# Performance work log

Measured on AMD Instinct MI355X. Metric: run time of the kernel, lower is better.

## Reference

```python
import jax, jax.numpy as jnp
import numpy as np
import math

NUM_HEADS = 16
SEGMENT_SIZE = 256
DILATION_RATE = 2


def _hilbert_curve(n):
    if n == 1:
        return [(0, 0)]
    m = n // 2
    sub = _hilbert_curve(m)
    pts = [(y, x) for (x, y) in sub]
    pts += [(x, y + m) for (x, y) in sub]
    pts += [(x + m, y + m) for (x, y) in sub]
    pts += [(m - 1 - y + m, m - 1 - x) for (x, y) in sub]
    return pts


def generate_hilbert_curve_mapping(seq_len):
    grid = 2 ** int(math.ceil(math.log2(math.sqrt(seq_len))))
    pts = _hilbert_curve(grid)
    lin2hil = np.zeros(seq_len, dtype=np.int32)
    for h_idx, (x, y) in enumerate(pts[:seq_len]):
        lin = y * grid + x
        if lin < seq_len:
            lin2hil[lin] = h_idx
    return lin2hil


def setup_inputs() -> dict:
    key = jax.random.key(0)
    k1, k2, k3 = jax.random.split(key, 3)
    B, S, H = 1, 4096, 2048
    scale = H ** -0.5
    x = jax.random.normal(k1, (B, S, H), dtype=jnp.float32)
    w_qkv = jax.random.normal(k2, (3 * H, H), dtype=jnp.float32) * scale
    w_out = jax.random.normal(k3, (H, H), dtype=jnp.float32) * scale
    hilbert_map = jnp.asarray(generate_hilbert_curve_mapping(S))
    return {"x": x, "w_qkv": w_qkv, "w_out": w_out, "hilbert_map": hilbert_map}


def _kv_positions(S, seg, dil):
    # Union of per-segment dilated positions: seg_start + j*dil (< segment end).
    seg_starts = np.arange(0, S, seg)
    within = np.arange(0, seg, dil)
    return jnp.asarray((seg_starts[:, None] + within[None, :]).reshape(-1))


def reference(x, w_qkv, w_out, hilbert_map):
    B, S, H = x.shape
    nh = NUM_HEADS
    hd = H // nh
    qkv = x @ w_qkv.T                              # [B,S,3H]
    qkv = qkv.reshape(B, S, 3, nh, hd).transpose(2, 0, 3, 1, 4)  # [3,B,nh,S,hd]
    q, k, v = qkv[0], qkv[1], qkv[2]

    kv_pos = _kv_positions(S, SEGMENT_SIZE, DILATION_RATE)  # [Nk]
    gathered = hilbert_map[kv_pos]                 # Hilbert-mapped KV indices
    kg = k[:, :, gathered, :]                      # [B,nh,Nk,hd]
    vg = v[:, :, gathered, :]

    scale = 1.0 / jnp.sqrt(jnp.float32(hd))
    scores = jnp.einsum("bhmd,bhnd->bhmn", q, kg) * scale
    p = jax.nn.softmax(scores, axis=-1)
    acc = jnp.einsum("bhmn,bhnd->bhmd", p, vg)     # [B,nh,S,hd]

    # Scatter: out[:, :, hilbert_map[m], :] = acc[:, :, m, :]
    out = jnp.zeros_like(acc).at[:, :, hilbert_map, :].set(acc)
    out = out.transpose(0, 2, 1, 3).reshape(B, S, H)
    return out @ w_out.T
```

## Files before the change

kernel.cpp:

```cpp
#include <hip/hip_runtime.h>
#include <math.h>

#define S_LEN 4096
#define HID   2048
#define NH    16
#define HD    128
#define NKV   2048
#define KT    64
#define QBLK  256
#define NT    (NKV / KT)
#define QSCALE 0.12754103668587426f

typedef __attribute__((ext_vector_type(8))) _Float16 half8;
typedef __attribute__((ext_vector_type(4))) _Float16 half4;
typedef __attribute__((ext_vector_type(2))) __fp16 fp16x2;
typedef __attribute__((ext_vector_type(4))) float f32x4;
typedef __attribute__((ext_vector_type(16))) float f32x16;

#define GLB_AS __attribute__((address_space(1)))
#define LDS_AS __attribute__((address_space(3)))

__device__ __forceinline__ void gload16(const void* g, void* l) {
  __builtin_amdgcn_global_load_lds((GLB_AS const void*)g, (LDS_AS void*)l, 16, 0, 0);
}

__device__ __forceinline__ unsigned pkrtz(float a, float b) {
  union { fp16x2 h; unsigned u; } cv;
  cv.h = __builtin_amdgcn_cvt_pkrtz(a, b);
  return cv.u;
}

__global__ void k_build_idx(const int* __restrict__ hmap, int* __restrict__ gidx) {
  int i = blockIdx.x * 256 + threadIdx.x;
  if (i < NKV) gidx[i] = hmap[2 * i];
}

__global__ void k_cvt_f16(const float* __restrict__ src, _Float16* __restrict__ dst, int n8) {
  int i = blockIdx.x * 256 + threadIdx.x;
  if (i < n8) {
    float4 a = ((const float4*)src)[2 * i];
    float4 b = ((const float4*)src)[2 * i + 1];
    half8 h;
    h[0] = (_Float16)a.x; h[1] = (_Float16)a.y; h[2] = (_Float16)a.z; h[3] = (_Float16)a.w;
    h[4] = (_Float16)b.x; h[5] = (_Float16)b.y; h[6] = (_Float16)b.z; h[7] = (_Float16)b.w;
    ((half8*)dst)[i] = h;
  }
}

template<bool OUT_F32>
__global__ __launch_bounds__(256)
void k_gemm2(const _Float16* __restrict__ A, const _Float16* __restrict__ B,
             void* __restrict__ Cv, int M, int N, int K,
             const int* __restrict__ arow)
{
  __shared__ __align__(16) char Asl[16384];
  __shared__ __align__(16) char Bsl[16384];
  const int tid = threadIdx.x;
  const int w = tid >> 6, lane = tid & 63;
  const int l15 = lane & 15, l4 = lane >> 4;
  const int m0 = blockIdx.y * 128, n0 = blockIdx.x * 128;
  const int wr = w >> 1, wc = w & 1;

  const int srow  = lane >> 3;
  const int kso   = ((lane & 7) ^ srow) * 8;
  const _Float16* Ap[4];
  const _Float16* Bp[4];
#pragma unroll
  for (int q = 0; q < 4; ++q) {
    int arel = m0 + 32 * w + 8 * q + srow;
    int ra = arow ? arow[arel] : arel;
    Ap[q] = A + (size_t)ra * K + kso;
    Bp[q] = B + (size_t)(n0 + 32 * w + 8 * q + srow) * K + kso;
  }

  f32x4 acc[4][4];
#pragma unroll
  for (int i = 0; i < 4; ++i)
#pragma unroll
    for (int j = 0; j < 4; ++j) acc[i][j] = (f32x4){0.f, 0.f, 0.f, 0.f};

#define STAGE_T(k0)                                                  \
  do {                                                               \
    _Pragma("unroll")                                                \
    for (int q = 0; q < 4; ++q) {                                    \
      gload16(Ap[q] + (k0), Asl + (4 * w + q) * 1024 + lane * 16);   \
      gload16(Bp[q] + (k0), Bsl + (4 * w + q) * 1024 + lane * 16);   \
    }                                                                \
  } while (0)

  STAGE_T(0);
  __syncthreads();

  const int nt = K >> 6;
  for (int t = 0; t < nt; ++t) {
    half8 af[4][2], bf[4][2];
#pragma unroll
    for (int mi = 0; mi < 4; ++mi) {
      int row = wr * 64 + mi * 16 + l15;
#pragma unroll
      for (int ks = 0; ks < 2; ++ks)
        af[mi][ks] = *(const half8*)(Asl + row * 128 + (((ks * 4 + l4) ^ (row & 7)) * 16));
    }
#pragma unroll
    for (int ni = 0; ni < 4; ++ni) {
      int row = wc * 64 + ni * 16 + l15;
#pragma unroll
      for (int ks = 0; ks < 2; ++ks)
        bf[ni][ks] = *(const half8*)(Bsl + row * 128 + (((ks * 4 + l4) ^ (row & 7)) * 16));
    }
    __syncthreads();
    if (t + 1 < nt) STAGE_T((t + 1) * 64);
    __builtin_amdgcn_s_setprio(1);
#pragma unroll
    for (int mi = 0; mi < 4; ++mi)
#pragma unroll
      for (int ni = 0; ni < 4; ++ni)
#pragma unroll
        for (int ks = 0; ks < 2; ++ks)
          acc[mi][ni] = __builtin_amdgcn_mfma_f32_16x16x32_f16(af[mi][ks], bf[ni][ks], acc[mi][ni], 0, 0, 0);
    __builtin_amdgcn_s_setprio(0);
    __syncthreads();
  }
#undef STAGE_T

  const int rbase = m0 + wr * 64 + l4 * 4;
  const int cbase = n0 + wc * 64 + l15;
#pragma unroll
  for (int mi = 0; mi < 4; ++mi)
#pragma unroll
    for (int ni = 0; ni < 4; ++ni)
#pragma unroll
      for (int e = 0; e < 4; ++e) {
        size_t idx = (size_t)(rbase + mi * 16 + e) * N + cbase + ni * 16;
        if (OUT_F32) ((float*)Cv)[idx] = acc[mi][ni][e];
        else ((_Float16*)Cv)[idx] = (_Float16)acc[mi][ni][e];
      }
}

__global__ __launch_bounds__(256)
void k_prep(const _Float16* __restrict__ kv, char* __restrict__ kimg,
            char* __restrict__ vtimg)
{
  __shared__ _Float16 Vs[64 * 136];
  const int tid = threadIdx.x;
  const int h = blockIdx.x >> 5;
  const int t = blockIdx.x & 31;
  const size_t ibase = (size_t)blockIdx.x * 16384;

#pragma unroll
  for (int it = 0; it < 4; ++it) {
    int idx = tid + 256 * it;
    int j = idx >> 4, dblk = idx & 15;
    const _Float16* rb = kv + (size_t)(t * KT + j) * (2 * HID) + h * HD + dblk * 8;
    half8 kvv = *(const half8*)rb;
    *(half8*)(kimg + ibase + ((j * 256 + 16 * dblk) ^ ((j & 7) << 4))) = kvv;
    half8 vv = *(const half8*)(rb + HID);
    *(half8*)(&Vs[j * 136 + dblk * 8]) = vv;
  }
  __syncthreads();
#pragma unroll
  for (int it = 0; it < 4; ++it) {
    int idx = tid + 256 * it;
    int jblk = idx >> 7, d = idx & 127;
    half8 o;
#pragma unroll
    for (int q = 0; q < 8; ++q) o[q] = Vs[(jblk * 8 + q) * 136 + d];
    *(half8*)(vtimg + ibase + ((d * 128 + 16 * jblk) ^ ((d & 7) << 4))) = o;
  }
}

__global__ __launch_bounds__(512, 2)
void k_attn4(const _Float16* __restrict__ qmat, const char* __restrict__ kimg,
             const char* __restrict__ vtimg, const int* __restrict__ hmap,
             _Float16* __restrict__ att)
{
  extern __shared__ __align__(16) char lds[];
  const int tid = threadIdx.x;
  const int w = tid >> 6, lane = tid & 63;
  const int l31 = lane & 31;
  const bool hi = (lane >> 5) != 0;
  const int hib = hi ? 1 : 0;
  const int work = (blockIdx.x & 7) * 32 + (blockIdx.x >> 3);
  const int h  = work >> 4;
  const int q0 = (work & 15) * QBLK;

  half8 qf[8];
  {
    const int qrow = q0 + w * 32 + l31;
    const _Float16* qb = qmat + (size_t)qrow * HID + h * HD + hib * 8;
    const _Float16 qs = (_Float16)QSCALE;
#pragma unroll
    for (int dk = 0; dk < 8; ++dk) {
      half8 v = *(const half8*)(qb + 16 * dk);
#pragma unroll
      for (int q = 0; q < 8; ++q) v[q] *= qs;
      qf[dk] = v;
    }
  }

  half8 ones;
#pragma unroll
  for (int q = 0; q < 8; ++q) ones[q] = (_Float16)1.0f;

  const char* kbase = kimg  + (size_t)h * NT * 16384;
  const char* vbase = vtimg + (size_t)h * NT * 16384;

  f32x16 acc[4];
  f32x16 accl;
#pragma unroll
  for (int dt = 0; dt < 4; ++dt)
#pragma unroll
    for (int r = 0; r < 16; ++r) acc[dt][r] = 0.f;
#pragma unroll
  for (int r = 0; r < 16; ++r) accl[r] = 0.f;
  float m = -1e30f;

#define STAGE(buf, t)                                                          \
  do {                                                                         \
    const char* ks_ = kbase + (size_t)(t) * 16384;                             \
    const char* vs_ = vbase + (size_t)(t) * 16384;                             \
    char* d_ = lds + (buf) * 32768;                                            \
    gload16(ks_ + w * 1024 + lane * 16,          d_ + w * 1024);               \
    gload16(ks_ + (8 + w) * 1024 + lane * 16,    d_ + (8 + w) * 1024);         \
    gload16(vs_ + w * 1024 + lane * 16,          d_ + 16384 + w * 1024);       \
    gload16(vs_ + (8 + w) * 1024 + lane * 16,    d_ + 16384 + (8 + w) * 1024); \
  } while (0)

  STAGE(0, 0);
  asm volatile("s_waitcnt vmcnt(0)");
  __syncthreads();

  int cur = 0;
  for (int t = 0; t < NT; ++t) {
    if (t + 1 < NT) STAGE(cur ^ 1, t + 1);
    const char* kl = lds + cur * 32768;
    const char* vl = kl + 16384;

    f32x16 s[2];
    __builtin_amdgcn_s_setprio(1);
#pragma unroll
    for (int jt = 0; jt < 2; ++jt) {
      f32x16 ss;
#pragma unroll
      for (int r = 0; r < 16; ++r) ss[r] = 0.f;
      const int j = jt * 32 + l31;
#pragma unroll
      for (int dk = 0; dk < 8; ++dk) {
        half8 kf = *(const half8*)(kl + j * 256 + ((dk * 32 + hib * 16) ^ ((l31 & 7) << 4)));
        ss = __builtin_amdgcn_mfma_f32_32x32x16_f16(kf, qf[dk], ss, 0, 0, 0);
      }
      s[jt] = ss;
    }
    __builtin_amdgcn_s_setprio(0);

    float vmax = -1e30f;
#pragma unroll
    for (int jt = 0; jt < 2; ++jt)
#pragma unroll
      for (int r = 0; r < 16; ++r) vmax = fmaxf(vmax, s[jt][r]);
    vmax = fmaxf(vmax, __shfl_xor(vmax, 32));

    if (__any(vmax > m + 8.f)) {
      float mn = fmaxf(m, vmax);
      float corr = exp2f(m - mn);
      m = mn;
#pragma unroll
      for (int dt = 0; dt < 4; ++dt)
#pragma unroll
        for (int r = 0; r < 16; ++r) acc[dt][r] *= corr;
#pragma unroll
      for (int r = 0; r < 16; ++r) accl[r] *= corr;
    }

    unsigned P_pk[2][4][2];
#pragma unroll
    for (int jt = 0; jt < 2; ++jt)
#pragma unroll
      for (int rq = 0; rq < 4; ++rq)
#pragma unroll
        for (int h2 = 0; h2 < 2; ++h2) {
          float p0 = exp2f(s[jt][4 * rq + 2 * h2]     - m);
          float p1 = exp2f(s[jt][4 * rq + 2 * h2 + 1] - m);
          P_pk[jt][rq][h2] = pkrtz(p0, p1);
        }

#pragma unroll
    for (int ks = 0; ks < 4; ++ks) {
      const int jt = ks >> 1, k1 = ks & 1;
      unsigned send0 = hi ? P_pk[jt][2 * k1][0]     : P_pk[jt][2 * k1 + 1][0];
      unsigned send1 = hi ? P_pk[jt][2 * k1][1]     : P_pk[jt][2 * k1 + 1][1];
      unsigned recv0 = (unsigned)__shfl_xor((int)send0, 32);
      unsigned recv1 = (unsigned)__shfl_xor((int)send1, 32);
      unsigned self0 = hi ? P_pk[jt][2 * k1 + 1][0] : P_pk[jt][2 * k1][0];
      unsigned self1 = hi ? P_pk[jt][2 * k1 + 1][1] : P_pk[jt][2 * k1][1];
      union { unsigned u[4]; half8 hv; } pf;
      pf.u[0] = hi ? recv0 : self0;
      pf.u[1] = hi ? recv1 : self1;
      pf.u[2] = hi ? self0 : recv0;
      pf.u[3] = hi ? self1 : recv1;
      __builtin_amdgcn_s_setprio(1);
#pragma unroll
      for (int dt = 0; dt < 4; ++dt) {
        const int d = dt * 32 + l31;
        half8 vf = *(const half8*)(vl + d * 128 + ((ks * 32 + hib * 16) ^ ((l31 & 7) << 4)));
        acc[dt] = __builtin_amdgcn_mfma_f32_32x32x16_f16(vf, pf.hv, acc[dt], 0, 0, 0);
      }
      accl = __builtin_amdgcn_mfma_f32_32x32x16_f16(ones, pf.hv, accl, 0, 0, 0);
      __builtin_amdgcn_s_setprio(0);
    }

    asm volatile("s_waitcnt vmcnt(0)");
    __syncthreads();
    cur ^= 1;
  }
#undef STAGE

  const float rl = 1.0f / accl[0];
  const int qrow = q0 + w * 32 + l31;
  const int srow = hmap[qrow];
  _Float16* ob = att + (size_t)srow * HID + h * HD;
#pragma unroll
  for (int dt = 0; dt < 4; ++dt)
#pragma unroll
    for (int rq = 0; rq < 4; ++rq) {
      const int d0 = dt * 32 + 8 * rq + 4 * hib;
      half4 o;
      o[0] = (_Float16)(acc[dt][4 * rq + 0] * rl);
      o[1] = (_Float16)(acc[dt][4 * rq + 1] * rl);
      o[2] = (_Float16)(acc[dt][4 * rq + 2] * rl);
      o[3] = (_Float16)(acc[dt][4 * rq + 3] * rl);
      *(half4*)(ob + d0) = o;
    }
}

extern "C" void kernel_launch(void* const* d_in, const int* in_sizes, int n_in,
                              void* d_out, int out_size, void* d_ws, size_t ws_size,
                              hipStream_t stream)
{
  const float* x     = (const float*)d_in[0];
  const float* w_qkv = (const float*)d_in[1];
  const float* w_out = (const float*)d_in[2];
  const int*   hmap  = (const int*)d_in[3];
  float* out = (float*)d_out;

  char* ws = (char*)d_ws;
  int* gidx = (int*)ws;                                          ws += 8192;
  _Float16* x16    = (_Float16*)ws;
  _Float16* att16  = (_Float16*)ws;                              ws += (size_t)S_LEN * HID * 2;
  _Float16* wqkv16 = (_Float16*)ws;                              ws += (size_t)3 * HID * HID * 2;
  _Float16* wout16 = (_Float16*)ws;                              ws += (size_t)HID * HID * 2;
  _Float16* q16    = (_Float16*)ws;                              ws += (size_t)S_LEN * HID * 2;
  _Float16* kv16   = (_Float16*)ws;                              ws += (size_t)NKV * 2 * HID * 2;
  char* kimg  = ws;                                              ws += (size_t)NH * NT * 16384;
  char* vtimg = ws;

  k_build_idx<<<8, 256, 0, stream>>>(hmap, gidx);

  k_cvt_f16<<<(S_LEN * HID / 8 + 255) / 256, 256, 0, stream>>>(x, x16, S_LEN * HID / 8);
  k_cvt_f16<<<(3 * HID * HID / 8 + 255) / 256, 256, 0, stream>>>(w_qkv, wqkv16, 3 * HID * HID / 8);
  k_cvt_f16<<<(HID * HID / 8 + 255) / 256, 256, 0, stream>>>(w_out, wout16, HID * HID / 8);

  dim3 gq(HID / 128, S_LEN / 128);
  k_gemm2<false><<<gq, 256, 0, stream>>>(x16, wqkv16, q16, S_LEN, HID, HID, nullptr);
  dim3 gkv(2 * HID / 128, NKV / 128);
  k_gemm2<false><<<gkv, 256, 0, stream>>>(x16, wqkv16 + (size_t)HID * HID, kv16,
                                          NKV, 2 * HID, HID, gidx);

  k_prep<<<NH * NT, 256, 0, stream>>>(kv16, kimg, vtimg);

  k_attn4<<<NH * (S_LEN / QBLK), 512, 65536, stream>>>(q16, kimg, vtimg, hmap, att16);

  dim3 go(HID / 128, S_LEN / 128);
  k_gemm2<true><<<go, 256, 0, stream>>>(att16, wout16, out, S_LEN, HID, HID, nullptr);
}
```

Before: 244.3 us.

## Fuse K/V image layout into KV GEMM epilogue and shrink attention blocks

The KV projection GEMM now writes its output straight into the swizzled K image and transposed V image, so the separate k_prep kernel and the kv16 intermediate buffer are gone. The attention kernel is re-tiled to 128 query rows per block with 256 threads, which doubles the grid and changes the LDS staging loop. The row-max reduction is also rewritten as a tree. The risk is that the scattered 2-byte stores in the GEMM epilogue are poorly coalesced, and the smaller attention blocks reuse each K/V tile less.

```diff
diff --git a/kernel.cpp b/kernel.cpp
--- a/kernel.cpp
+++ b/kernel.cpp
@@ -7,7 +7,7 @@
 #define HD    128
 #define NKV   2048
 #define KT    64
-#define QBLK  256
+#define QBLK  128
 #define NT    (NKV / KT)
 #define QSCALE 0.12754103668587426f
 
@@ -47,11 +47,12 @@
   }
 }
 
-template<bool OUT_F32>
+template<int MODE>
 __global__ __launch_bounds__(256)
 void k_gemm2(const _Float16* __restrict__ A, const _Float16* __restrict__ B,
              void* __restrict__ Cv, int M, int N, int K,
-             const int* __restrict__ arow)
+             const int* __restrict__ arow,
+             char* __restrict__ kimg, char* __restrict__ vtimg)
 {
   __shared__ __align__(16) char Asl[16384];
   __shared__ __align__(16) char Bsl[16384];
@@ -131,46 +132,31 @@
     for (int ni = 0; ni < 4; ++ni)
 #pragma unroll
       for (int e = 0; e < 4; ++e) {
-        size_t idx = (size_t)(rbase + mi * 16 + e) * N + cbase + ni * 16;
-        if (OUT_F32) ((float*)Cv)[idx] = acc[mi][ni][e];
-        else ((_Float16*)Cv)[idx] = (_Float16)acc[mi][ni][e];
+        int row = rbase + mi * 16 + e;
+        int col = cbase + ni * 16;
+        if (MODE == 1) {
+          ((float*)Cv)[(size_t)row * N + col] = acc[mi][ni][e];
+        } else if (MODE == 0) {
+          ((_Float16*)Cv)[(size_t)row * N + col] = (_Float16)acc[mi][ni][e];
+        } else {
+          _Float16 val = (_Float16)acc[mi][ni][e];
+          int t = row >> 6, j = row & 63;
+          if (col < HID) {
+            int h = col >> 7, d = col & 127;
+            int off = (h * 32 + t) * 16384 + ((j * 256 + 2 * d) ^ ((j & 7) << 4));
+            *(_Float16*)(kimg + off) = val;
+          } else {
+            int nn = col - HID;
+            int h = nn >> 7, d = nn & 127;
+            int off = (h * 32 + t) * 16384 + ((d * 128 + 2 * j) ^ ((d & 7) << 4));
+            *(_Float16*)(vtimg + off) = val;
+          }
+        }
       }
 }
 
-__global__ __launch_bounds__(256)
-void k_prep(const _Float16* __restrict__ kv, char* __restrict__ kimg,
-            char* __restrict__ vtimg)
-{
-  __shared__ _Float16 Vs[64 * 136];
-  const int tid = threadIdx.x;
-  const int h = blockIdx.x >> 5;
-  const int t = blockIdx.x & 31;
-  const size_t ibase = (size_t)blockIdx.x * 16384;
-
-#pragma unroll
-  for (int it = 0; it < 4; ++it) {
-    int idx = tid + 256 * it;
-    int j = idx >> 4, dblk = idx & 15;
-    const _Float16* rb = kv + (size_t)(t * KT + j) * (2 * HID) + h * HD + dblk * 8;
-    half8 kvv = *(const half8*)rb;
-    *(half8*)(kimg + ibase + ((j * 256 + 16 * dblk) ^ ((j & 7) << 4))) = kvv;
-    half8 vv = *(const half8*)(rb + HID);
-    *(half8*)(&Vs[j * 136 + dblk * 8]) = vv;
-  }
-  __syncthreads();
-#pragma unroll
-  for (int it = 0; it < 4; ++it) {
-    int idx = tid + 256 * it;
-    int jblk = idx >> 7, d = idx & 127;
-    half8 o;
-#pragma unroll
-    for (int q = 0; q < 8; ++q) o[q] = Vs[(jblk * 8 + q) * 136 + d];
-    *(half8*)(vtimg + ibase + ((d * 128 + 16 * jblk) ^ ((d & 7) << 4))) = o;
-  }
-}
-
-__global__ __launch_bounds__(512, 2)
-void k_attn4(const _Float16* __restrict__ qmat, const char* __restrict__ kimg,
+__global__ __launch_bounds__(256, 2)
+void k_attn5(const _Float16* __restrict__ qmat, const char* __restrict__ kimg,
              const char* __restrict__ vtimg, const int* __restrict__ hmap,
              _Float16* __restrict__ att)
 {
@@ -180,9 +166,9 @@
   const int l31 = lane & 31;
   const bool hi = (lane >> 5) != 0;
   const int hib = hi ? 1 : 0;
-  const int work = (blockIdx.x & 7) * 32 + (blockIdx.x >> 3);
-  const int h  = work >> 4;
-  const int q0 = (work & 15) * QBLK;
+  const int work = (blockIdx.x & 7) * 64 + (blockIdx.x >> 3);
+  const int h  = work >> 5;
+  const int q0 = (work & 31) * QBLK;
 
   half8 qf[8];
   {
@@ -220,10 +206,12 @@
     const char* ks_ = kbase + (size_t)(t) * 16384;                             \
     const char* vs_ = vbase + (size_t)(t) * 16384;                             \
     char* d_ = lds + (buf) * 32768;                                            \
-    gload16(ks_ + w * 1024 + lane * 16,          d_ + w * 1024);               \
-    gload16(ks_ + (8 + w) * 1024 + lane * 16,    d_ + (8 + w) * 1024);         \
-    gload16(vs_ + w * 1024 + lane * 16,          d_ + 16384 + w * 1024);       \
-    gload16(vs_ + (8 + w) * 1024 + lane * 16,    d_ + 16384 + (8 + w) * 1024); \
+    _Pragma("unroll")                                                          \
+    for (int g = 0; g < 4; ++g) {                                              \
+      gload16(ks_ + (4 * w + g) * 1024 + lane * 16, d_ + (4 * w + g) * 1024);  \
+      gload16(vs_ + (4 * w + g) * 1024 + lane * 16,                            \
+              d_ + 16384 + (4 * w + g) * 1024);                                \
+    }                                                                          \
   } while (0)
 
   STAGE(0, 0);
@@ -253,11 +241,13 @@
     }
     __builtin_amdgcn_s_setprio(0);
 
-    float vmax = -1e30f;
-#pragma unroll
-    for (int jt = 0; jt < 2; ++jt)
-#pragma unroll
-      for (int r = 0; r < 16; ++r) vmax = fmaxf(vmax, s[jt][r]);
+    float t8[8];
+#pragma unroll
+    for (int r = 0; r < 8; ++r)
+      t8[r] = fmaxf(fmaxf(s[0][r], s[0][r + 8]), fmaxf(s[1][r], s[1][r + 8]));
+    float ta = fmaxf(fmaxf(t8[0], t8[1]), fmaxf(t8[2], t8[3]));
+    float tb = fmaxf(fmaxf(t8[4], t8[5]), fmaxf(t8[6], t8[7]));
+    float vmax = fmaxf(ta, tb);
     vmax = fmaxf(vmax, __shfl_xor(vmax, 32));
 
     if (__any(vmax > m + 8.f)) {
@@ -350,7 +340,6 @@
   _Float16* wqkv16 = (_Float16*)ws;                              ws += (size_t)3 * HID * HID * 2;
   _Float16* wout16 = (_Float16*)ws;                              ws += (size_t)HID * HID * 2;
   _Float16* q16    = (_Float16*)ws;                              ws += (size_t)S_LEN * HID * 2;
-  _Float16* kv16   = (_Float16*)ws;                              ws += (size_t)NKV * 2 * HID * 2;
   char* kimg  = ws;                                              ws += (size_t)NH * NT * 16384;
   char* vtimg = ws;
 
@@ -361,15 +350,13 @@
   k_cvt_f16<<<(HID * HID / 8 + 255) / 256, 256, 0, stream>>>(w_out, wout16, HID * HID / 8);
 
   dim3 gq(HID / 128, S_LEN / 128);
-  k_gemm2<false><<<gq, 256, 0, stream>>>(x16, wqkv16, q16, S_LEN, HID, HID, nullptr);
+  k_gemm2<0><<<gq, 256, 0, stream>>>(x16, wqkv16, q16, S_LEN, HID, HID, nullptr, nullptr, nullptr);
   dim3 gkv(2 * HID / 128, NKV / 128);
-  k_gemm2<false><<<gkv, 256, 0, stream>>>(x16, wqkv16 + (size_t)HID * HID, kv16,
-                                          NKV, 2 * HID, HID, gidx);
-
-  k_prep<<<NH * NT, 256, 0, stream>>>(kv16, kimg, vtimg);
-
-  k_attn4<<<NH * (S_LEN / QBLK), 512, 65536, stream>>>(q16, kimg, vtimg, hmap, att16);
+  k_gemm2<2><<<gkv, 256, 0, stream>>>(x16, wqkv16 + (size_t)HID * HID, nullptr,
+                                      NKV, 2 * HID, HID, gidx, kimg, vtimg);
+
+  k_attn5<<<NH * (S_LEN / QBLK), 256, 65536, stream>>>(q16, kimg, vtimg, hmap, att16);
 
   dim3 go(HID / 128, S_LEN / 128);
-  k_gemm2<true><<<go, 256, 0, stream>>>(att16, wout16, out, S_LEN, HID, HID, nullptr);
-}
+  k_gemm2<1><<<go, 256, 0, stream>>>(att16, wout16, out, S_LEN, HID, HID, nullptr, nullptr, nullptr);
+}
```

Measured after the change: 249.0 us. Within noise of the previous version (+1.9%).
